# Kernel optimization log

Hardware: AMD Instinct MI355X
Metric: run time of the kernel (lower is better)

The kernel has to match this reference:

```python
import jax, jax.numpy as jnp
import numpy as np

H, W = 512, 512          # resized_height, resized_width
R = 2                    # cdist norm order
B, NGT = 4, 64
MAX_DIST = float(np.sqrt(H ** 2 + W ** 2))
EPS = 1e-6


def setup_inputs() -> dict:
    key = jax.random.key(0)
    k1, k2, k3, k4 = jax.random.split(key, 4)
    prob_map = jax.random.uniform(k1, (B, H, W), dtype=jnp.float32)
    # all entries > 0.2 so the torch filter prob_y[prob_y>0.2] keeps every point
    prob_y = 0.2 + 0.79 * jax.random.uniform(k2, (B, NGT), dtype=jnp.float32)
    gt = jax.random.uniform(k3, (B, NGT, 2), dtype=jnp.float32) * jnp.array([H - 1, W - 1], jnp.float32)
    orig_sizes = jax.random.randint(k4, (B, 2), 512, 2048, dtype=jnp.int32)
    return {"prob_map": prob_map, "prob_y": prob_y, "gt": gt, "orig_sizes": orig_sizes}


def _pixel_locations():
    # cartesian([arange(H), arange(W)]) -> (H*W, 2), row-major
    ii, jj = jnp.meshgrid(jnp.arange(H), jnp.arange(W), indexing="ij")
    return jnp.stack([ii, jj], axis=-1).reshape(-1, 2).astype(jnp.float32)


def _ghd(prob_map, prob_y, gt, orig_sizes):
    locs = _pixel_locations()                      # (P, 2), P = H*W
    resized = jnp.array([H, W], jnp.float32)

    def per_batch(pm, py, g, osz):
        nf = osz.astype(jnp.float32) / resized     # (2,) norm factor
        nx = nf * locs                             # (P, 2)
        ny = nf * g                                # (G, 2)
        diff = jnp.abs(nx[:, None, :] - ny[None, :, :])   # (P, G, 2)
        d = jnp.sum(diff ** R, axis=-1) ** (1.0 / R)      # (P, G)
        p = pm.reshape(-1)                         # (P,)
        n_est_pts = jnp.sum(p)
        n_gt_sum = jnp.sum(jnp.where(py > 0.2, py, 0.0))
        weighted = p[:, None] * py[None, :] * d    # p_x * p_y * d
        term_1 = jnp.sum(jnp.min(weighted, axis=1)) / (n_est_pts + EPS)
        dense = (1.0 - p[:, None]) * MAX_DIST + weighted
        term_2 = jnp.sum(jnp.min(dense, axis=0)) / (n_gt_sum + EPS)
        return term_1, term_2

    t1, t2 = jax.vmap(per_batch)(prob_map, prob_y, gt, orig_sizes)
    return t1.mean() + t2.mean()


def reference(prob_map, prob_y, gt, orig_sizes):
    return _ghd(prob_map, prob_y, gt, orig_sizes)
```

## Files before the change

kernel.cpp:

```cpp
#include <hip/hip_runtime.h>
#include <math.h>

#define HH 512
#define WW 512
#define PP (HH * WW)
#define GG 64
#define BB 4
#define THREADS 256
#define NA 64
#define NB 128
#define TILE 1024
#define NTILES (PP / TILE)
#define MAX_DIST 724.0773439350246f
#define EPSV 1e-6f


__global__ void ghd_init(float* __restrict__ ws) {
    int t = threadIdx.x;
    if (t < 8) ws[t] = 0.0f;
    unsigned* gm = reinterpret_cast<unsigned*>(ws) + 8;
    if (t < BB * GG) gm[t] = 0x7f7fffffu;
}

__launch_bounds__(THREADS)
__global__ void ghd_main(const float* __restrict__ prob_map,
                         const float* __restrict__ prob_y,
                         const float* __restrict__ gt,
                         const int*   __restrict__ osz,
                         float*       __restrict__ ws) {
    const int b    = blockIdx.y;
    const int tid  = threadIdx.x;
    const int lane = tid & 63;
    const int wave = tid >> 6;

    __shared__ float4   sdat[TILE];
    __shared__ unsigned sgmin[GG];
    __shared__ float    s_t1[4], s_ne[4];

    const float nf0 = (float)osz[2 * b]     * (1.0f / HH);
    const float nf1 = (float)osz[2 * b + 1] * (1.0f / WW);
    const float* __restrict__ pm = prob_map + (size_t)b * PP;

    if (blockIdx.x < NA) {
        if (tid < GG) {
            float py = prob_y[b * GG + tid];
            sdat[tid] = make_float4(nf0 * gt[(b * GG + tid) * 2],
                                    nf1 * gt[(b * GG + tid) * 2 + 1],
                                    py, py * py);
        }
        __syncthreads();

        float t1 = 0.0f, ne = 0.0f;
        const float4* __restrict__ pm4 = (const float4*)pm;
#pragma unroll
        for (int c = 0; c < 4; ++c) {
            int   idx4 = (c * NA + blockIdx.x) * THREADS + tid;
            float4 p4  = pm4[idx4];
            int   pid  = idx4 * 4;
            float nx0  = nf0 * (float)(pid >> 9);
            float j0   = (float)(pid & (WW - 1));
            float nx1a = nf1 * j0;
            float nx1b = nf1 * (j0 + 1.0f);
            float nx1c = nf1 * (j0 + 2.0f);
            float nx1d = nf1 * (j0 + 3.0f);
            float ma = 3.4e38f, mb = 3.4e38f, mc = 3.4e38f, md = 3.4e38f;
#pragma unroll 16
            for (int g = 0; g < GG; ++g) {
                float4 gd  = sdat[g];
                float  dx  = nx0 - gd.x;
                float  dx2 = dx * dx;
                float  da = nx1a - gd.y, db = nx1b - gd.y;
                float  dc = nx1c - gd.y, dd = nx1d - gd.y;
                ma = fminf(ma, gd.w * fmaf(da, da, dx2));
                mb = fminf(mb, gd.w * fmaf(db, db, dx2));
                mc = fminf(mc, gd.w * fmaf(dc, dc, dx2));
                md = fminf(md, gd.w * fmaf(dd, dd, dx2));
            }
            t1 += p4.x * __builtin_amdgcn_sqrtf(ma) + p4.y * __builtin_amdgcn_sqrtf(mb)
                + p4.z * __builtin_amdgcn_sqrtf(mc) + p4.w * __builtin_amdgcn_sqrtf(md);
            ne += p4.x + p4.y + p4.z + p4.w;
        }
#pragma unroll
        for (int off = 1; off < 64; off <<= 1) {
            t1 += __shfl_xor(t1, off);
            ne += __shfl_xor(ne, off);
        }
        if (lane == 0) { s_t1[wave] = t1; s_ne[wave] = ne; }
        __syncthreads();
        if (tid == 0) {
            atomicAdd(&ws[b],     s_t1[0] + s_t1[1] + s_t1[2] + s_t1[3]);
            atomicAdd(&ws[4 + b], s_ne[0] + s_ne[1] + s_ne[2] + s_ne[3]);
        }
    } else {
        if (tid < GG) sgmin[tid] = 0x7f7fffffu;
        const int g  = lane;
        const float gx = nf0 * gt[(b * GG + g) * 2];
        const float gy = nf1 * gt[(b * GG + g) * 2 + 1];
        const float py = prob_y[b * GG + g];
        float gmin = 3.4e38f;

        const int bx = blockIdx.x - NA;
        for (int t = bx; t < NTILES; t += NB) {
            __syncthreads();
#pragma unroll
            for (int i = tid; i < TILE; i += THREADS) {
                int   pid = t * TILE + i;
                float p   = pm[pid];
                sdat[i] = make_float4(nf0 * (float)(pid >> 9),
                                      nf1 * (float)(pid & (WW - 1)),
                                      p,
                                      fmaf(-p, MAX_DIST, MAX_DIST));
            }
            __syncthreads();
            const float4* __restrict__ mytile = sdat + wave * (TILE / 4);
#pragma unroll 8
            for (int k = 0; k < TILE / 4; ++k) {
                float4 px = mytile[k];
                float  dx = px.x - gx, dy = px.y - gy;
                float  d  = __builtin_amdgcn_sqrtf(fmaf(dx, dx, dy * dy));
                gmin = fminf(gmin, fmaf(px.z * py, d, px.w));
            }
        }
        atomicMin(&sgmin[g], __float_as_uint(gmin));
        __syncthreads();
        if (tid < GG) {
            unsigned* gm = reinterpret_cast<unsigned*>(ws) + 8;
            atomicMin(gm + b * GG + tid, sgmin[tid]);
        }
    }
}

__global__ void ghd_final(const float* __restrict__ prob_y,
                          const float* __restrict__ ws,
                          float*       __restrict__ out) {
    const int tid = threadIdx.x;
    const int b = tid >> 6;
    const int g = tid & 63;
    const unsigned* gm = reinterpret_cast<const unsigned*>(ws) + 8;

    float mv  = __uint_as_float(gm[b * GG + g]);
    float py  = prob_y[b * GG + g];
    float pyf = (py > 0.2f) ? py : 0.0f;
#pragma unroll
    for (int off = 1; off < 64; off <<= 1) {
        mv  += __shfl_xor(mv, off);
        pyf += __shfl_xor(pyf, off);
    }
    __shared__ float res[4];
    if (g == 0) {
        float term1 = ws[b] / (ws[4 + b] + EPSV);
        float term2 = mv    / (pyf       + EPSV);
        res[b] = term1 + term2;
    }
    __syncthreads();
    if (tid == 0) out[0] = 0.25f * (res[0] + res[1] + res[2] + res[3]);
}

extern "C" void kernel_launch(void* const* d_in, const int* in_sizes, int n_in,
                              void* d_out, int out_size, void* d_ws, size_t ws_size,
                              hipStream_t stream) {
    const float* prob_map = (const float*)d_in[0];
    const float* prob_y   = (const float*)d_in[1];
    const float* gt       = (const float*)d_in[2];
    const int*   osz      = (const int*)d_in[3];
    float* out = (float*)d_out;
    float* ws  = (float*)d_ws;

    ghd_init<<<1, 256, 0, stream>>>(ws);
    dim3 grid(NA + NB, BB);
    ghd_main<<<grid, 256, 0, stream>>>(prob_map, prob_y, gt, osz, ws);
    ghd_final<<<1, 256, 0, stream>>>(prob_y, ws, out);
}
```

Baseline: 88.66 us.

## Fuse term1/term2 into one pass per tile with early-out skip and no atomics

Each block now handles one 1024-pixel tile. It loads the pixels once, computes the per-pixel min over the GTs for term 1, then reuses the same shared tile for the per-GT min for term 2. The term-2 loop skips groups of four pixels when the wave's running min is already below their lower bound (1-p)*MAX_DIST. Atomics and the init kernel are replaced by per-tile partial results in the workspace, reduced in the final kernel. This removes a launch and the duplicate loads, but it adds a larger final reduction and divergence-dependent skipping.

New measurement: 125.3 us. +41.3%, slower.

```diff
diff --git a/kernel.cpp b/kernel.cpp
--- a/kernel.cpp
+++ b/kernel.cpp
@@ -7,20 +7,11 @@
 #define GG 64
 #define BB 4
 #define THREADS 256
-#define NA 64
-#define NB 128
 #define TILE 1024
-#define NTILES (PP / TILE)
+#define NT (PP / TILE)
 #define MAX_DIST 724.0773439350246f
 #define EPSV 1e-6f
 
-
-__global__ void ghd_init(float* __restrict__ ws) {
-    int t = threadIdx.x;
-    if (t < 8) ws[t] = 0.0f;
-    unsigned* gm = reinterpret_cast<unsigned*>(ws) + 8;
-    if (t < BB * GG) gm[t] = 0x7f7fffffu;
-}
 
 __launch_bounds__(THREADS)
 __global__ void ghd_main(const float* __restrict__ prob_map,
@@ -28,105 +19,102 @@
                          const float* __restrict__ gt,
                          const int*   __restrict__ osz,
                          float*       __restrict__ ws) {
+    const int t    = blockIdx.x;
     const int b    = blockIdx.y;
     const int tid  = threadIdx.x;
     const int lane = tid & 63;
     const int wave = tid >> 6;
 
-    __shared__ float4   sdat[TILE];
-    __shared__ unsigned sgmin[GG];
-    __shared__ float    s_t1[4], s_ne[4];
+    __shared__ float4 gdat[GG];
+    __shared__ float4 sdat[TILE];
+    __shared__ float  wmin[4][GG];
+    __shared__ float  s_t1[4], s_ne[4];
 
     const float nf0 = (float)osz[2 * b]     * (1.0f / HH);
     const float nf1 = (float)osz[2 * b + 1] * (1.0f / WW);
-    const float* __restrict__ pm = prob_map + (size_t)b * PP;
 
-    if (blockIdx.x < NA) {
-        if (tid < GG) {
-            float py = prob_y[b * GG + tid];
-            sdat[tid] = make_float4(nf0 * gt[(b * GG + tid) * 2],
-                                    nf1 * gt[(b * GG + tid) * 2 + 1],
-                                    py, py * py);
+    if (tid < GG) {
+        float py = prob_y[b * GG + tid];
+        gdat[tid] = make_float4(nf0 * gt[(b * GG + tid) * 2],
+                                nf1 * gt[(b * GG + tid) * 2 + 1],
+                                py, py * py);
+    }
+
+    const int   pid0 = t * TILE + tid * 4;
+    const float4 p4  = ((const float4*)(prob_map + (size_t)b * PP))[pid0 >> 2];
+    const float nx0  = nf0 * (float)(pid0 >> 9);
+    const float j0   = (float)(pid0 & (WW - 1));
+    const float nx1a = nf1 * j0;
+    const float nx1b = nf1 * (j0 + 1.0f);
+    const float nx1c = nf1 * (j0 + 2.0f);
+    const float nx1d = nf1 * (j0 + 3.0f);
+    const float bsa = fmaf(-p4.x, MAX_DIST, MAX_DIST);
+    const float bsb = fmaf(-p4.y, MAX_DIST, MAX_DIST);
+    const float bsc = fmaf(-p4.z, MAX_DIST, MAX_DIST);
+    const float bsd = fmaf(-p4.w, MAX_DIST, MAX_DIST);
+    sdat[tid * 4 + 0] = make_float4(nx0, nx1a, p4.x, bsa);
+    sdat[tid * 4 + 1] = make_float4(nx0, nx1b, p4.y, bsb);
+    sdat[tid * 4 + 2] = make_float4(nx0, nx1c, p4.z, bsc);
+    sdat[tid * 4 + 3] = make_float4(nx0, nx1d, p4.w, bsd);
+    __syncthreads();
+
+    float ma = 3.4e38f, mb = 3.4e38f, mc = 3.4e38f, md = 3.4e38f;
+#pragma unroll 16
+    for (int g = 0; g < GG; ++g) {
+        float4 gd  = gdat[g];
+        float  dx  = nx0 - gd.x;
+        float  dx2 = dx * dx;
+        float  da = nx1a - gd.y, db = nx1b - gd.y;
+        float  dc = nx1c - gd.y, dd = nx1d - gd.y;
+        ma = fminf(ma, gd.w * fmaf(da, da, dx2));
+        mb = fminf(mb, gd.w * fmaf(db, db, dx2));
+        mc = fminf(mc, gd.w * fmaf(dc, dc, dx2));
+        md = fminf(md, gd.w * fmaf(dd, dd, dx2));
+    }
+    float t1 = p4.x * __builtin_amdgcn_sqrtf(ma) + p4.y * __builtin_amdgcn_sqrtf(mb)
+             + p4.z * __builtin_amdgcn_sqrtf(mc) + p4.w * __builtin_amdgcn_sqrtf(md);
+    float ne = p4.x + p4.y + p4.z + p4.w;
+
+    const float4 gme = gdat[lane];
+    float gmin = 3.4e38f;
+    const float4* __restrict__ tp = &sdat[wave * (TILE / 4)];
+#pragma unroll 4
+    for (int k = 0; k < TILE / 4; k += 4) {
+        float4 x0 = tp[k], x1 = tp[k + 1], x2 = tp[k + 2], x3 = tp[k + 3];
+        float mbse = fminf(fminf(x0.w, x1.w), fminf(x2.w, x3.w));
+        if (!__all(mbse >= gmin)) {
+            float d0x = x0.x - gme.x, d0y = x0.y - gme.y;
+            float d1x = x1.x - gme.x, d1y = x1.y - gme.y;
+            float d2x = x2.x - gme.x, d2y = x2.y - gme.y;
+            float d3x = x3.x - gme.x, d3y = x3.y - gme.y;
+            float e0 = __builtin_amdgcn_sqrtf(fmaf(d0x, d0x, d0y * d0y));
+            float e1 = __builtin_amdgcn_sqrtf(fmaf(d1x, d1x, d1y * d1y));
+            float e2 = __builtin_amdgcn_sqrtf(fmaf(d2x, d2x, d2y * d2y));
+            float e3 = __builtin_amdgcn_sqrtf(fmaf(d3x, d3x, d3y * d3y));
+            gmin = fminf(gmin, fmaf(x0.z * gme.z, e0, x0.w));
+            gmin = fminf(gmin, fmaf(x1.z * gme.z, e1, x1.w));
+            gmin = fminf(gmin, fmaf(x2.z * gme.z, e2, x2.w));
+            gmin = fminf(gmin, fmaf(x3.z * gme.z, e3, x3.w));
         }
-        __syncthreads();
+    }
+    wmin[wave][lane] = gmin;
 
-        float t1 = 0.0f, ne = 0.0f;
-        const float4* __restrict__ pm4 = (const float4*)pm;
 #pragma unroll
-        for (int c = 0; c < 4; ++c) {
-            int   idx4 = (c * NA + blockIdx.x) * THREADS + tid;
-            float4 p4  = pm4[idx4];
-            int   pid  = idx4 * 4;
-            float nx0  = nf0 * (float)(pid >> 9);
-            float j0   = (float)(pid & (WW - 1));
-            float nx1a = nf1 * j0;
-            float nx1b = nf1 * (j0 + 1.0f);
-            float nx1c = nf1 * (j0 + 2.0f);
-            float nx1d = nf1 * (j0 + 3.0f);
-            float ma = 3.4e38f, mb = 3.4e38f, mc = 3.4e38f, md = 3.4e38f;
-#pragma unroll 16
-            for (int g = 0; g < GG; ++g) {
-                float4 gd  = sdat[g];
-                float  dx  = nx0 - gd.x;
-                float  dx2 = dx * dx;
-                float  da = nx1a - gd.y, db = nx1b - gd.y;
-                float  dc = nx1c - gd.y, dd = nx1d - gd.y;
-                ma = fminf(ma, gd.w * fmaf(da, da, dx2));
-                mb = fminf(mb, gd.w * fmaf(db, db, dx2));
-                mc = fminf(mc, gd.w * fmaf(dc, dc, dx2));
-                md = fminf(md, gd.w * fmaf(dd, dd, dx2));
-            }
-            t1 += p4.x * __builtin_amdgcn_sqrtf(ma) + p4.y * __builtin_amdgcn_sqrtf(mb)
-                + p4.z * __builtin_amdgcn_sqrtf(mc) + p4.w * __builtin_amdgcn_sqrtf(md);
-            ne += p4.x + p4.y + p4.z + p4.w;
-        }
-#pragma unroll
-        for (int off = 1; off < 64; off <<= 1) {
-            t1 += __shfl_xor(t1, off);
-            ne += __shfl_xor(ne, off);
-        }
-        if (lane == 0) { s_t1[wave] = t1; s_ne[wave] = ne; }
-        __syncthreads();
-        if (tid == 0) {
-            atomicAdd(&ws[b],     s_t1[0] + s_t1[1] + s_t1[2] + s_t1[3]);
-            atomicAdd(&ws[4 + b], s_ne[0] + s_ne[1] + s_ne[2] + s_ne[3]);
-        }
-    } else {
-        if (tid < GG) sgmin[tid] = 0x7f7fffffu;
-        const int g  = lane;
-        const float gx = nf0 * gt[(b * GG + g) * 2];
-        const float gy = nf1 * gt[(b * GG + g) * 2 + 1];
-        const float py = prob_y[b * GG + g];
-        float gmin = 3.4e38f;
+    for (int off = 1; off < 64; off <<= 1) {
+        t1 += __shfl_xor(t1, off);
+        ne += __shfl_xor(ne, off);
+    }
+    if (lane == 0) { s_t1[wave] = t1; s_ne[wave] = ne; }
+    __syncthreads();
 
-        const int bx = blockIdx.x - NA;
-        for (int t = bx; t < NTILES; t += NB) {
-            __syncthreads();
-#pragma unroll
-            for (int i = tid; i < TILE; i += THREADS) {
-                int   pid = t * TILE + i;
-                float p   = pm[pid];
-                sdat[i] = make_float4(nf0 * (float)(pid >> 9),
-                                      nf1 * (float)(pid & (WW - 1)),
-                                      p,
-                                      fmaf(-p, MAX_DIST, MAX_DIST));
-            }
-            __syncthreads();
-            const float4* __restrict__ mytile = sdat + wave * (TILE / 4);
-#pragma unroll 8
-            for (int k = 0; k < TILE / 4; ++k) {
-                float4 px = mytile[k];
-                float  dx = px.x - gx, dy = px.y - gy;
-                float  d  = __builtin_amdgcn_sqrtf(fmaf(dx, dx, dy * dy));
-                gmin = fminf(gmin, fmaf(px.z * py, d, px.w));
-            }
-        }
-        atomicMin(&sgmin[g], __float_as_uint(gmin));
-        __syncthreads();
-        if (tid < GG) {
-            unsigned* gm = reinterpret_cast<unsigned*>(ws) + 8;
-            atomicMin(gm + b * GG + tid, sgmin[tid]);
-        }
+    if (tid == 0) {
+        ws[b * NT + t]        = s_t1[0] + s_t1[1] + s_t1[2] + s_t1[3];
+        ws[1024 + b * NT + t] = s_ne[0] + s_ne[1] + s_ne[2] + s_ne[3];
+    }
+    if (tid < GG) {
+        float v = fminf(fminf(wmin[0][tid], wmin[1][tid]),
+                        fminf(wmin[2][tid], wmin[3][tid]));
+        ws[2048 + (b * NT + t) * GG + tid] = v;
     }
 }
 
@@ -136,22 +124,29 @@
     const int tid = threadIdx.x;
     const int b = tid >> 6;
     const int g = tid & 63;
-    const unsigned* gm = reinterpret_cast<const unsigned*>(ws) + 8;
 
-    float mv  = __uint_as_float(gm[b * GG + g]);
+    float mv = 3.4e38f;
+    const float* gp = ws + 2048 + b * NT * GG + g;
+#pragma unroll 8
+    for (int t = 0; t < NT; ++t) mv = fminf(mv, gp[t * GG]);
+
     float py  = prob_y[b * GG + g];
     float pyf = (py > 0.2f) ? py : 0.0f;
+
+    float4 tv = ((const float4*)(ws + b * NT))[g];
+    float4 nv = ((const float4*)(ws + 1024 + b * NT))[g];
+    float t1s = tv.x + tv.y + tv.z + tv.w;
+    float nes = nv.x + nv.y + nv.z + nv.w;
+
 #pragma unroll
     for (int off = 1; off < 64; off <<= 1) {
         mv  += __shfl_xor(mv, off);
         pyf += __shfl_xor(pyf, off);
+        t1s += __shfl_xor(t1s, off);
+        nes += __shfl_xor(nes, off);
     }
     __shared__ float res[4];
-    if (g == 0) {
-        float term1 = ws[b] / (ws[4 + b] + EPSV);
-        float term2 = mv    / (pyf       + EPSV);
-        res[b] = term1 + term2;
-    }
+    if (g == 0) res[b] = t1s / (nes + EPSV) + mv / (pyf + EPSV);
     __syncthreads();
     if (tid == 0) out[0] = 0.25f * (res[0] + res[1] + res[2] + res[3]);
 }
@@ -166,8 +161,7 @@
     float* out = (float*)d_out;
     float* ws  = (float*)d_ws;
 
-    ghd_init<<<1, 256, 0, stream>>>(ws);
-    dim3 grid(NA + NB, BB);
-    ghd_main<<<grid, 256, 0, stream>>>(prob_map, prob_y, gt, osz, ws);
+    dim3 grid(NT, BB);
+    ghd_main<<<grid, THREADS, 0, stream>>>(prob_map, prob_y, gt, osz, ws);
     ghd_final<<<1, 256, 0, stream>>>(prob_y, ws, out);
 }
```
